# Optimization experiments

Hardware: AMD Instinct MI355X
Metric: run time of the kernel (lower is better)

The kernel has to match this reference:

```python
import jax, jax.numpy as jnp
import numpy as np

N_NODES = 50000
N_EDGES = 600000
IN_DIM = 4
HID = 128
N_LAYERS = 6
BN_EPS = 1e-5


def setup_inputs() -> dict:
    key = jax.random.key(0)
    ks = jax.random.split(key, 20)
    x = jax.random.normal(ks[0], (N_NODES, IN_DIM), dtype=jnp.float32)
    edge_index = jax.random.randint(ks[1], (2, N_EDGES), 0, N_NODES, dtype=jnp.int32)
    s = 0.05
    return {
        "x": x,
        "edge_index": edge_index,
        "enc_w": jax.random.normal(ks[2], (IN_DIM, HID), jnp.float32) * s,
        "enc_b": jnp.zeros((HID,), jnp.float32),
        "enc_bn_g": jnp.ones((HID,), jnp.float32),
        "enc_bn_b": jnp.zeros((HID,), jnp.float32),
        "conv_w": jax.random.normal(ks[3], (N_LAYERS, HID, HID), jnp.float32) * s,
        "conv_b": jnp.zeros((N_LAYERS, HID), jnp.float32),
        "bn_g": jnp.ones((N_LAYERS, HID), jnp.float32),
        "bn_b": jnp.zeros((N_LAYERS, HID), jnp.float32),
        "dec_w1": jax.random.normal(ks[4], (HID, HID // 2), jnp.float32) * s,
        "dec_b1": jnp.zeros((HID // 2,), jnp.float32),
        "dec_w2": jax.random.normal(ks[5], (HID // 2, HID // 4), jnp.float32) * s,
        "dec_b2": jnp.zeros((HID // 4,), jnp.float32),
        "dec_w3": jax.random.normal(ks[6], (HID // 4, 1), jnp.float32) * s,
        "dec_b3": jnp.zeros((1,), jnp.float32),
    }


def _batchnorm(h, g, b):
    # training-mode BatchNorm1d over node axis (biased variance, like torch)
    mu = h.mean(axis=0)
    var = jnp.mean(jnp.square(h - mu), axis=0)
    return (h - mu) * jax.lax.rsqrt(var + BN_EPS) * g + b


def _gcn_conv(h, W, b, src, dst, inv_sqrt_deg, n):
    # PyG GCNConv: sym-normalized A+I aggregation, aggregate at dst
    hw = h @ W                                   # [N, HID]
    norm = inv_sqrt_deg[src] * inv_sqrt_deg[dst]  # [E]
    msg = hw[src] * norm[:, None]                # [E, HID] (dominant traffic)
    agg = jax.ops.segment_sum(msg, dst, num_segments=n)
    self_loop = hw * jnp.square(inv_sqrt_deg)[:, None]
    return agg + self_loop + b


def reference(x, edge_index, enc_w, enc_b, enc_bn_g, enc_bn_b,
              conv_w, conv_b, bn_g, bn_b,
              dec_w1, dec_b1, dec_w2, dec_b2, dec_w3, dec_b3):
    n = x.shape[0]
    src, dst = edge_index[0], edge_index[1]
    # degree includes self loop (A + I)
    deg = jax.ops.segment_sum(jnp.ones_like(dst, dtype=x.dtype), dst, num_segments=n) + 1.0
    inv_sqrt_deg = jax.lax.rsqrt(deg)

    # encoder: Linear -> ReLU -> BatchNorm (dropout = identity in eval)
    h = jax.nn.relu(x @ enc_w + enc_b)
    h = _batchnorm(h, enc_bn_g, enc_bn_b)

    for l in range(N_LAYERS):
        h_new = _gcn_conv(h, conv_w[l], conv_b[l], src, dst, inv_sqrt_deg, n)
        h_new = jax.nn.relu(_batchnorm(h_new, bn_g[l], bn_b[l]))
        h = h + h_new  # residual

    # decoder MLP
    d = jax.nn.relu(h @ dec_w1 + dec_b1)
    d = jax.nn.relu(d @ dec_w2 + dec_b2)
    out = d @ dec_w3 + dec_b3
    return out.squeeze(-1)  # [N]
```

## Files before the change

### kernel.cpp

```cpp
#include <hip/hip_runtime.h>

#define BN_EPS 1e-5f

typedef unsigned int uint_t;
typedef unsigned short ushort_t;
typedef short bf16x8 __attribute__((ext_vector_type(8)));
typedef float f32x4 __attribute__((ext_vector_type(4)));

__device__ __forceinline__ float bflo(uint_t v) { return __uint_as_float(v << 16); }
__device__ __forceinline__ float bfhi(uint_t v) { return __uint_as_float(v & 0xffff0000u); }
__device__ __forceinline__ uint_t f2bf(float f) {
    uint_t u = __float_as_uint(f);
    u += 0x7fffu + ((u >> 16) & 1u);
    return u >> 16;
}

__device__ __forceinline__ void acc8(float* a, uint4 g, float w) {
    a[0] = fmaf(bflo(g.x), w, a[0]);
    a[1] = fmaf(bfhi(g.x), w, a[1]);
    a[2] = fmaf(bflo(g.y), w, a[2]);
    a[3] = fmaf(bfhi(g.y), w, a[3]);
    a[4] = fmaf(bflo(g.z), w, a[4]);
    a[5] = fmaf(bfhi(g.z), w, a[5]);
    a[6] = fmaf(bflo(g.w), w, a[6]);
    a[7] = fmaf(bfhi(g.w), w, a[7]);
}


__global__ void count_kernel(const int* __restrict__ ei, int* __restrict__ counts, int E) {
    int e = blockIdx.x * blockDim.x + threadIdx.x;
    if (e < E) atomicAdd(&counts[ei[E + e]], 1);
}

__global__ __launch_bounds__(256) void scan_part(const int* __restrict__ counts,
                                                 int* __restrict__ rowptr, int* __restrict__ bsum,
                                                 float* __restrict__ isd, int n) {
    const int tid = threadIdx.x;
    const int lane = tid & 63, wave = tid >> 6;
    __shared__ int wsum[4];
    int idx0 = blockIdx.x * 2048 + tid * 8;
    int v[8];
    int tsum = 0;
#pragma unroll
    for (int j = 0; j < 8; j++) {
        int i = idx0 + j;
        int c = (i < n) ? counts[i] : 0;
        if (i < n) isd[i] = rsqrtf((float)c + 1.0f);
        v[j] = (i < n) ? (((c + 4) >> 2) << 2) : 0;
        tsum += v[j];
    }
    int incl = tsum;
#pragma unroll
    for (int off = 1; off < 64; off <<= 1) {
        int t = __shfl_up(incl, off, 64);
        if (lane >= off) incl += t;
    }
    if (lane == 63) wsum[wave] = incl;
    __syncthreads();
    int wexcl = 0;
    for (int w2 = 0; w2 < wave; w2++) wexcl += wsum[w2];
    int run = wexcl + (incl - tsum);
#pragma unroll
    for (int j = 0; j < 8; j++) {
        int i = idx0 + j;
        if (i < n) rowptr[i] = run;
        run += v[j];
    }
    if (tid == 255) bsum[blockIdx.x] = run;
}

__global__ void scan_mid(int* __restrict__ bsum, int nb) {
    int lane = threadIdx.x;
    int v = (lane < nb) ? bsum[lane] : 0;
    int incl = v;
#pragma unroll
    for (int off = 1; off < 64; off <<= 1) {
        int t = __shfl_up(incl, off, 64);
        if (lane >= off) incl += t;
    }
    if (lane < nb) bsum[lane] = incl - v;
    if (lane == 63) bsum[nb] = incl;
}

__global__ void scan_add_self(int* __restrict__ rowptr, const int* __restrict__ bsum,
                              const int* __restrict__ counts, const float* __restrict__ isd,
                              int* __restrict__ cursor, int2* __restrict__ edges, int n, int nb) {
    int i = blockIdx.x * 256 + threadIdx.x;
    if (i < n) {
        int rp = rowptr[i] + bsum[i >> 11];
        rowptr[i] = rp;
        cursor[i] = rp;
        int c = counts[i];
        int pos = rp + c;
        int end = rp + (((c + 4) >> 2) << 2);
        float v = isd[i];
        edges[pos] = make_int2(i, __float_as_int(v * v));
        for (int p = pos + 1; p < end; p++) edges[p] = make_int2(i, 0);
    } else if (i == n) {
        rowptr[n] = bsum[nb];
    }
}

__global__ void scatter_kernel(const int* __restrict__ ei, int* __restrict__ cursor,
                               const float* __restrict__ isd, int2* __restrict__ edges, int E) {
    int e = blockIdx.x * blockDim.x + threadIdx.x;
    if (e < E) {
        int s = ei[e], d = ei[E + e];
        int idx = atomicAdd(&cursor[d], 1);
        edges[idx] = make_int2(s, __float_as_int(isd[s] * isd[d]));
    }
}


__global__ void wtrans_kernel(const float* __restrict__ W, ushort_t* __restrict__ Wt) {
    int id = blockIdx.x * 256 + threadIdx.x;
    int l = id >> 14, rem = id & 16383;
    int k = rem >> 7, n = rem & 127;
    Wt[(l << 14) + (n << 7) + k] = f2bf(W[id]);
}


__global__ __launch_bounds__(256) void encoder_kernel(const float* __restrict__ x,
                                                      const float* __restrict__ W,
                                                      const float* __restrict__ b,
                                                      float* __restrict__ h0,
                                                      float* __restrict__ stats, int N) {
    int tid = threadIdx.x;
    int g = blockIdx.x * 256 + tid;
    int total = gridDim.x * 256;
    int c = tid & 127;
    float w0 = W[c], w1 = W[128 + c], w2 = W[256 + c], w3 = W[384 + c], bb = b[c];
    float s = 0.f, q = 0.f;
    int tot = N * 128;
    for (int i = g; i < tot; i += total) {
        int n = i >> 7;
        float4 xv = ((const float4*)x)[n];
        float v = fmaf(xv.x, w0, fmaf(xv.y, w1, fmaf(xv.z, w2, fmaf(xv.w, w3, bb))));
        v = fmaxf(v, 0.f);
        h0[i] = v;
        s += v;
        q += v * v;
    }
    __shared__ float ls[256];
    ls[tid] = s;
    __syncthreads();
    if (tid < 128) atomicAdd(&stats[tid], ls[tid] + ls[tid + 128]);
    __syncthreads();
    ls[tid] = q;
    __syncthreads();
    if (tid < 128) atomicAdd(&stats[128 + tid], ls[tid] + ls[tid + 128]);
}


#define SWZ(byte, row) ((byte) ^ (((row) & 7) << 4))

template <int MODE>
__global__ __launch_bounds__(512) void mfma_gemm(const float* __restrict__ h,
                                                 const ushort_t* __restrict__ aggb,
                                                 const float* __restrict__ stats,
                                                 const float* __restrict__ g,
                                                 const float* __restrict__ beta, float invN,
                                                 const ushort_t* __restrict__ Wt,
                                                 float* __restrict__ hout,
                                                 ushort_t* __restrict__ hwb, int N) {
    __shared__ ushort_t As[128 * 128];
    __shared__ float s_sc[128], s_sh[128];
    const int tid = threadIdx.x;
    const int row0 = blockIdx.x * 128;

    if (tid < 128) {
        float S = stats[tid], Q = stats[tid + 128];
        float mu = S * invN;
        float var = fmaxf(Q * invN - mu * mu, 0.f);
        float rs = rsqrtf(var + BN_EPS);
        float sc = g[tid] * rs;
        s_sc[tid] = sc;
        s_sh[tid] = beta[tid] - mu * sc;
    }
    __syncthreads();

#pragma unroll
    for (int j = 0; j < 4; j++) {
        int idx = (j * 512 + tid) * 8;
        int r = idx >> 7, c = idx & 127;
        int grow = row0 + r;
        float av[8] = {0.f, 0.f, 0.f, 0.f, 0.f, 0.f, 0.f, 0.f};
        if (grow < N) {
            float4 h0 = *(const float4*)&h[(size_t)grow * 128 + c];
            float4 h1 = *(const float4*)&h[(size_t)grow * 128 + c + 4];
            float hv[8] = {h0.x, h0.y, h0.z, h0.w, h1.x, h1.y, h1.z, h1.w};
            if (MODE == 0) {
#pragma unroll
                for (int k = 0; k < 8; k++) av[k] = fmaf(hv[k], s_sc[c + k], s_sh[c + k]);
            } else {
                uint4 ag = *(const uint4*)&aggb[(size_t)grow * 128 + c];
                float ga[8] = {bflo(ag.x), bfhi(ag.x), bflo(ag.y), bfhi(ag.y),
                               bflo(ag.z), bfhi(ag.z), bflo(ag.w), bfhi(ag.w)};
#pragma unroll
                for (int k = 0; k < 8; k++)
                    av[k] = hv[k] + fmaxf(fmaf(ga[k], s_sc[c + k], s_sh[c + k]), 0.f);
            }
            *(float4*)&hout[(size_t)grow * 128 + c] = make_float4(av[0], av[1], av[2], av[3]);
            *(float4*)&hout[(size_t)grow * 128 + c + 4] = make_float4(av[4], av[5], av[6], av[7]);
        }
        uint4 p;
        p.x = f2bf(av[0]) | (f2bf(av[1]) << 16);
        p.y = f2bf(av[2]) | (f2bf(av[3]) << 16);
        p.z = f2bf(av[4]) | (f2bf(av[5]) << 16);
        p.w = f2bf(av[6]) | (f2bf(av[7]) << 16);
        *(uint4*)((char*)As + SWZ(r * 256 + c * 2, r)) = p;
    }
    __syncthreads();

    const int w = tid >> 6, l = tid & 63;
    const int mrow = l & 15, kg = l >> 4;
    const int arow = w * 16 + mrow;
    bf16x8 afr[4];
#pragma unroll
    for (int ks = 0; ks < 4; ks++)
        afr[ks] = *(const bf16x8*)((const char*)As + SWZ(arow * 256 + ks * 64 + kg * 16, arow));

    f32x4 acc[8];
#pragma unroll
    for (int nt = 0; nt < 8; nt++) acc[nt] = (f32x4){0.f, 0.f, 0.f, 0.f};

#pragma unroll
    for (int nt = 0; nt < 8; nt++) {
        const ushort_t* wp = &Wt[(size_t)(nt * 16 + mrow) * 128 + kg * 8];
#pragma unroll
        for (int ks = 0; ks < 4; ks++) {
            bf16x8 bfr = *(const bf16x8*)&wp[ks * 32];
            acc[nt] = __builtin_amdgcn_mfma_f32_16x16x32_bf16(afr[ks], bfr, acc[nt], 0, 0, 0);
        }
    }

#pragma unroll
    for (int nt = 0; nt < 8; nt++) {
#pragma unroll
        for (int r = 0; r < 4; r++) {
            int grow = row0 + w * 16 + kg * 4 + r;
            if (grow < N) hwb[(size_t)grow * 128 + nt * 16 + mrow] = f2bf(acc[nt][r]);
        }
    }
}


__global__ __launch_bounds__(256) void dec1_kernel(const float* __restrict__ A0,
                                                   const ushort_t* __restrict__ aggb,
                                                   const float* __restrict__ stats,
                                                   const float* __restrict__ g,
                                                   const float* __restrict__ beta, float invN,
                                                   const float* __restrict__ B,
                                                   const float* __restrict__ bias,
                                                   float* __restrict__ Cf, int N) {
    constexpr int K = 128, NOUT = 64, TN = NOUT / 16;
    constexpr int LDA = K + 1;
    __shared__ float As[64 * LDA];
    __shared__ float Bs[16 * NOUT];
    __shared__ float s_sc[128], s_sh[128];
    const int tid = threadIdx.x;
    const int row0 = blockIdx.x * 64;

    if (tid < 128) {
        float S = stats[tid], Q = stats[tid + 128];
        float mu = S * invN;
        float var = fmaxf(Q * invN - mu * mu, 0.f);
        float rs = rsqrtf(var + BN_EPS);
        float sc = g[tid] * rs;
        s_sc[tid] = sc;
        s_sh[tid] = beta[tid] - mu * sc;
    }
    __syncthreads();
#pragma unroll
    for (int j = 0; j < 4; j++) {
        int idx = (j * 256 + tid) * 8;
        int r = idx >> 7, c = idx & 127;
        int grow = row0 + r;
        float av[8] = {0.f, 0.f, 0.f, 0.f, 0.f, 0.f, 0.f, 0.f};
        if (grow < N) {
            float4 h0 = *(const float4*)&A0[(size_t)grow * 128 + c];
            float4 h1 = *(const float4*)&A0[(size_t)grow * 128 + c + 4];
            float hv[8] = {h0.x, h0.y, h0.z, h0.w, h1.x, h1.y, h1.z, h1.w};
            uint4 ag = *(const uint4*)&aggb[(size_t)grow * 128 + c];
            float ga[8] = {bflo(ag.x), bfhi(ag.x), bflo(ag.y), bfhi(ag.y),
                           bflo(ag.z), bfhi(ag.z), bflo(ag.w), bfhi(ag.w)};
#pragma unroll
            for (int k = 0; k < 8; k++)
                av[k] = hv[k] + fmaxf(fmaf(ga[k], s_sc[c + k], s_sh[c + k]), 0.f);
        }
#pragma unroll
        for (int k = 0; k < 8; k++) As[r * LDA + c + k] = av[k];
    }
    __syncthreads();

    float acc[4][TN];
#pragma unroll
    for (int i = 0; i < 4; i++)
#pragma unroll
        for (int j = 0; j < TN; j++) acc[i][j] = 0.f;

    const int tx = tid & 15, ty = tid >> 4;
    for (int k0 = 0; k0 < K; k0 += 16) {
        for (int f = tid; f < 16 * NOUT / 4; f += 256) {
            int r = f / (NOUT / 4), c4 = (f % (NOUT / 4)) * 4;
            *(float4*)&Bs[r * NOUT + c4] = *(const float4*)&B[(size_t)(k0 + r) * NOUT + c4];
        }
        __syncthreads();
#pragma unroll
        for (int kk = 0; kk < 16; ++kk) {
            float a[4], bf[TN];
#pragma unroll
            for (int i = 0; i < 4; i++) a[i] = As[(ty * 4 + i) * LDA + k0 + kk];
#pragma unroll
            for (int j = 0; j < TN; j++) bf[j] = Bs[kk * NOUT + tx * TN + j];
#pragma unroll
            for (int i = 0; i < 4; i++)
#pragma unroll
                for (int j = 0; j < TN; j++) acc[i][j] = fmaf(a[i], bf[j], acc[i][j]);
        }
        __syncthreads();
    }

#pragma unroll
    for (int i = 0; i < 4; i++) {
        int grow = row0 + ty * 4 + i;
        if (grow >= N) continue;
#pragma unroll
        for (int j = 0; j < TN; j++) {
            int c = tx * TN + j;
            Cf[(size_t)grow * NOUT + c] = fmaxf(acc[i][j] + bias[c], 0.f);
        }
    }
}


__global__ __launch_bounds__(256) void dec23_kernel(const float* __restrict__ d1,
                                                    const float* __restrict__ dw2,
                                                    const float* __restrict__ db2,
                                                    const float* __restrict__ dw3,
                                                    const float* __restrict__ db3,
                                                    float* __restrict__ out, int N) {
    constexpr int K = 64, NOUT = 32, TN = 2;
    __shared__ float As[64 * (K + 1)];
    __shared__ float Bs[K * NOUT];
    __shared__ float t2[64 * 33];
    __shared__ float w3s[32];
    const int tid = threadIdx.x;
    const int row0 = blockIdx.x * 64;

    if (tid < 32) w3s[tid] = dw3[tid];
#pragma unroll
    for (int j = 0; j < 4; j++) {
        int idx = (j * 256 + tid) * 4;
        int r = idx >> 6, c = idx & 63;
        int grow = row0 + r;
        float4 a = make_float4(0.f, 0.f, 0.f, 0.f);
        if (grow < N) a = *(const float4*)&d1[(size_t)grow * K + c];
        As[r * (K + 1) + c + 0] = a.x;
        As[r * (K + 1) + c + 1] = a.y;
        As[r * (K + 1) + c + 2] = a.z;
        As[r * (K + 1) + c + 3] = a.w;
    }
#pragma unroll
    for (int j = 0; j < 2; j++) {
        int f = (j * 256 + tid) * 4;
        *(float4*)&Bs[f] = *(const float4*)&dw2[f];
    }
    __syncthreads();

    const int tx = tid & 15, ty = tid >> 4;
    float acc[4][TN];
#pragma unroll
    for (int i = 0; i < 4; i++)
#pragma unroll
        for (int j = 0; j < TN; j++) acc[i][j] = 0.f;
#pragma unroll
    for (int kk = 0; kk < K; ++kk) {
        float a[4], bf[TN];
#pragma unroll
        for (int i = 0; i < 4; i++) a[i] = As[(ty * 4 + i) * (K + 1) + kk];
#pragma unroll
        for (int j = 0; j < TN; j++) bf[j] = Bs[kk * NOUT + tx * TN + j];
#pragma unroll
        for (int i = 0; i < 4; i++)
#pragma unroll
            for (int j = 0; j < TN; j++) acc[i][j] = fmaf(a[i], bf[j], acc[i][j]);
    }
#pragma unroll
    for (int i = 0; i < 4; i++) {
#pragma unroll
        for (int j = 0; j < TN; j++) {
            int c = tx * TN + j;
            t2[(ty * 4 + i) * 33 + c] = fmaxf(acc[i][j] + db2[c], 0.f);
        }
    }
    __syncthreads();
    if (tid < 64) {
        int n = row0 + tid;
        if (n < N) {
            float s = db3[0];
#pragma unroll
            for (int k = 0; k < 32; k++) s = fmaf(t2[tid * 33 + k], w3s[k], s);
            out[n] = s;
        }
    }
}


__global__ __launch_bounds__(256) void agg_kernel(const ushort_t* __restrict__ hwb,
                                                  const int* __restrict__ rowptr,
                                                  const int2* __restrict__ edges,
                                                  ushort_t* __restrict__ aggb,
                                                  float* __restrict__ stats, int N) {
    const int tid = threadIdx.x;
    const int wave = tid >> 6, lane = tid & 63;
    const int cbase = (lane & 15) * 8;
    const int gid = blockIdx.x * 16 + (tid >> 4);
    const int G = gridDim.x * 16;
    float s[8], q[8];
#pragma unroll
    for (int j = 0; j < 8; j++) {
        s[j] = 0.f;
        q[j] = 0.f;
    }

    for (int n = gid; n < N; n += G) {
        const int e0 = rowptr[n], e1 = rowptr[n + 1];
        float a[8] = {0.f, 0.f, 0.f, 0.f, 0.f, 0.f, 0.f, 0.f};
        for (int e = e0; e < e1; e += 16) {
            int c0 = min(e, e1 - 4);
            int c1 = min(e + 4, e1 - 4);
            int c2 = min(e + 8, e1 - 4);
            int c3 = min(e + 12, e1 - 4);
            int4 p0a = *(const int4*)&edges[c0];
            int4 p0b = *(const int4*)&edges[c0 + 2];
            int4 p1a = *(const int4*)&edges[c1];
            int4 p1b = *(const int4*)&edges[c1 + 2];
            int4 p2a = *(const int4*)&edges[c2];
            int4 p2b = *(const int4*)&edges[c2 + 2];
            int4 p3a = *(const int4*)&edges[c3];
            int4 p3b = *(const int4*)&edges[c3 + 2];
            float4 wv0 = make_float4(__int_as_float(p0a.y), __int_as_float(p0a.w),
                                     __int_as_float(p0b.y), __int_as_float(p0b.w));
            float4 wv1 = make_float4(__int_as_float(p1a.y), __int_as_float(p1a.w),
                                     __int_as_float(p1b.y), __int_as_float(p1b.w));
            float4 wv2 = make_float4(__int_as_float(p2a.y), __int_as_float(p2a.w),
                                     __int_as_float(p2b.y), __int_as_float(p2b.w));
            float4 wv3 = make_float4(__int_as_float(p3a.y), __int_as_float(p3a.w),
                                     __int_as_float(p3b.y), __int_as_float(p3b.w));
            if (e + 4 >= e1) wv1 = make_float4(0.f, 0.f, 0.f, 0.f);
            if (e + 8 >= e1) wv2 = make_float4(0.f, 0.f, 0.f, 0.f);
            if (e + 12 >= e1) wv3 = make_float4(0.f, 0.f, 0.f, 0.f);
            uint4 g0 = *(const uint4*)&hwb[(size_t)p0a.x * 128 + cbase];
            uint4 g1 = *(const uint4*)&hwb[(size_t)p0a.z * 128 + cbase];
            uint4 g2 = *(const uint4*)&hwb[(size_t)p0b.x * 128 + cbase];
            uint4 g3 = *(const uint4*)&hwb[(size_t)p0b.z * 128 + cbase];
            uint4 g4 = *(const uint4*)&hwb[(size_t)p1a.x * 128 + cbase];
            uint4 g5 = *(const uint4*)&hwb[(size_t)p1a.z * 128 + cbase];
            uint4 g6 = *(const uint4*)&hwb[(size_t)p1b.x * 128 + cbase];
            uint4 g7 = *(const uint4*)&hwb[(size_t)p1b.z * 128 + cbase];
            uint4 g8 = *(const uint4*)&hwb[(size_t)p2a.x * 128 + cbase];
            uint4 g9 = *(const uint4*)&hwb[(size_t)p2a.z * 128 + cbase];
            uint4 g10 = *(const uint4*)&hwb[(size_t)p2b.x * 128 + cbase];
            uint4 g11 = *(const uint4*)&hwb[(size_t)p2b.z * 128 + cbase];
            uint4 g12 = *(const uint4*)&hwb[(size_t)p3a.x * 128 + cbase];
            uint4 g13 = *(const uint4*)&hwb[(size_t)p3a.z * 128 + cbase];
            uint4 g14 = *(const uint4*)&hwb[(size_t)p3b.x * 128 + cbase];
            uint4 g15 = *(const uint4*)&hwb[(size_t)p3b.z * 128 + cbase];
            acc8(a, g0, wv0.x);
            acc8(a, g1, wv0.y);
            acc8(a, g2, wv0.z);
            acc8(a, g3, wv0.w);
            acc8(a, g4, wv1.x);
            acc8(a, g5, wv1.y);
            acc8(a, g6, wv1.z);
            acc8(a, g7, wv1.w);
            acc8(a, g8, wv2.x);
            acc8(a, g9, wv2.y);
            acc8(a, g10, wv2.z);
            acc8(a, g11, wv2.w);
            acc8(a, g12, wv3.x);
            acc8(a, g13, wv3.y);
            acc8(a, g14, wv3.z);
            acc8(a, g15, wv3.w);
        }
        uint4 p;
        p.x = f2bf(a[0]) | (f2bf(a[1]) << 16);
        p.y = f2bf(a[2]) | (f2bf(a[3]) << 16);
        p.z = f2bf(a[4]) | (f2bf(a[5]) << 16);
        p.w = f2bf(a[6]) | (f2bf(a[7]) << 16);
        *(uint4*)&aggb[(size_t)n * 128 + cbase] = p;
#pragma unroll
        for (int j = 0; j < 8; j++) {
            s[j] += a[j];
            q[j] += a[j] * a[j];
        }
    }

#pragma unroll
    for (int j = 0; j < 8; j++) {
        s[j] += __shfl_xor(s[j], 16, 64);
        s[j] += __shfl_xor(s[j], 32, 64);
        q[j] += __shfl_xor(q[j], 16, 64);
        q[j] += __shfl_xor(q[j], 32, 64);
    }
    __shared__ float ls[4][128];
    if (lane < 16) {
#pragma unroll
        for (int j = 0; j < 8; j++) ls[wave][cbase + j] = s[j];
    }
    __syncthreads();
    if (tid < 128) atomicAdd(&stats[tid], ls[0][tid] + ls[1][tid] + ls[2][tid] + ls[3][tid]);
    __syncthreads();
    if (lane < 16) {
#pragma unroll
        for (int j = 0; j < 8; j++) ls[wave][cbase + j] = q[j];
    }
    __syncthreads();
    if (tid < 128) atomicAdd(&stats[128 + tid], ls[0][tid] + ls[1][tid] + ls[2][tid] + ls[3][tid]);
}


extern "C" void kernel_launch(void* const* d_in, const int* in_sizes, int n_in, void* d_out,
                              int out_size, void* d_ws, size_t ws_size, hipStream_t stream) {
    const float* x = (const float*)d_in[0];
    const int* ei = (const int*)d_in[1];
    const float* enc_w = (const float*)d_in[2];
    const float* enc_b = (const float*)d_in[3];
    const float* enc_bn_g = (const float*)d_in[4];
    const float* enc_bn_b = (const float*)d_in[5];
    const float* conv_w = (const float*)d_in[6];
    const float* bn_g = (const float*)d_in[8];
    const float* bn_b = (const float*)d_in[9];
    const float* dw1 = (const float*)d_in[10];
    const float* db1 = (const float*)d_in[11];
    const float* dw2 = (const float*)d_in[12];
    const float* db2 = (const float*)d_in[13];
    const float* dw3 = (const float*)d_in[14];
    const float* db3 = (const float*)d_in[15];
    float* out = (float*)d_out;

    const int N = in_sizes[0] / 4;
    const int E = in_sizes[1] / 2;
    const size_t N128 = (size_t)N * 128;
    const float invN = 1.0f / N;

    float* h = (float*)d_ws;
    ushort_t* aggb = (ushort_t*)(h + N128);
    ushort_t* hwb = aggb + N128;
    ushort_t* wt = hwb + N128;
    float* stats = (float*)(wt + 6 * 16384);
    float* isd = stats + 7 * 256;
    int* counts = (int*)(isd + N);
    int* rowptr = counts + N;
    int* cursor = rowptr + N + 1;
    int* bsum = cursor + N;
    int2* edges = (int2*)(((uintptr_t)(bsum + 66) + 15) & ~(uintptr_t)15);
    float* d1 = (float*)hwb;
    float* d2 = (float*)aggb;

    (void)hipMemsetAsync(stats, 0, 7 * 256 * sizeof(float), stream);
    (void)hipMemsetAsync(counts, 0, (size_t)N * sizeof(int), stream);

    const int eb = (E + 255) / 256;
    const int snb = (N + 2047) / 2048;
    count_kernel<<<eb, 256, 0, stream>>>(ei, counts, E);
    scan_part<<<snb, 256, 0, stream>>>(counts, rowptr, bsum, isd, N);
    scan_mid<<<1, 64, 0, stream>>>(bsum, snb);
    scan_add_self<<<(N + 256) / 256, 256, 0, stream>>>(rowptr, bsum, counts, isd, cursor, edges,
                                                       N, snb);
    scatter_kernel<<<eb, 256, 0, stream>>>(ei, cursor, isd, edges, E);
    wtrans_kernel<<<384, 256, 0, stream>>>(conv_w, wt);

    encoder_kernel<<<1024, 256, 0, stream>>>(x, enc_w, enc_b, h, stats, N);

    const int mblocks = (N + 127) / 128;
    const int gblocks = (N + 63) / 64;
    const int ablocks = 768;

    mfma_gemm<0><<<mblocks, 512, 0, stream>>>(h, nullptr, stats, enc_bn_g, enc_bn_b, invN, wt, h,
                                              hwb, N);
    agg_kernel<<<ablocks, 256, 0, stream>>>(hwb, rowptr, edges, aggb, stats + 256, N);

    for (int l = 1; l < 6; l++) {
        mfma_gemm<1><<<mblocks, 512, 0, stream>>>(h, aggb, stats + l * 256, bn_g + (l - 1) * 128,
                                                  bn_b + (l - 1) * 128, invN,
                                                  wt + (size_t)l * 16384, h, hwb, N);
        agg_kernel<<<ablocks, 256, 0, stream>>>(hwb, rowptr, edges, aggb, stats + (l + 1) * 256,
                                                N);
    }

    dec1_kernel<<<gblocks, 256, 0, stream>>>(h, aggb, stats + 6 * 256, bn_g + 5 * 128,
                                             bn_b + 5 * 128, invN, dw1, db1, d1, N);
    dec23_kernel<<<gblocks, 256, 0, stream>>>(d1, dw2, db2, dw3, db3, out, N);
    (void)d2;
}
```

Baseline: 531.3 us.

## Fuse all GCN layer GEMM and aggregation stages into one cooperative persistent kernel

Replaces the twelve per-layer launches of the MFMA GEMM and aggregation kernels with a single cooperative kernel that loops over the six layers and uses grid-wide syncs between phases. The GEMM tile shrinks to 64 rows per 256-thread block and is processed in a grid-stride loop, and the aggregation runs in the same persistent blocks. The goal is to remove kernel launch gaps and tail effects. In exchange it adds grid.sync barriers, caps the grid by occupancy, and may lower per-phase parallelism or raise register pressure because two phases share one kernel.

New measurement: 1.403 ms. 164% more time.

```diff
diff --git a/kernel.cpp b/kernel.cpp
--- a/kernel.cpp
+++ b/kernel.cpp
@@ -1,4 +1,7 @@
 #include <hip/hip_runtime.h>
+#include <hip/hip_cooperative_groups.h>
+
+namespace cg = cooperative_groups;
 
 #define BN_EPS 1e-5f
 
@@ -110,7 +113,6 @@
         edges[idx] = make_int2(s, __float_as_int(isd[s] * isd[d]));
     }
 }
-
 
 __global__ void wtrans_kernel(const float* __restrict__ W, ushort_t* __restrict__ Wt) {
     int id = blockIdx.x * 256 + threadIdx.x;
@@ -154,93 +156,215 @@
 
 #define SWZ(byte, row) ((byte) ^ (((row) & 7) << 4))
 
-template <int MODE>
-__global__ __launch_bounds__(512) void mfma_gemm(const float* __restrict__ h,
-                                                 const ushort_t* __restrict__ aggb,
-                                                 const float* __restrict__ stats,
-                                                 const float* __restrict__ g,
-                                                 const float* __restrict__ beta, float invN,
-                                                 const ushort_t* __restrict__ Wt,
-                                                 float* __restrict__ hout,
-                                                 ushort_t* __restrict__ hwb, int N) {
-    __shared__ ushort_t As[128 * 128];
+__global__ __launch_bounds__(256, 4) void layers_kernel(
+    float* __restrict__ h, ushort_t* __restrict__ aggb, ushort_t* __restrict__ hwb,
+    const ushort_t* __restrict__ wt, float* __restrict__ stats, const float* __restrict__ enc_g,
+    const float* __restrict__ enc_bt, const float* __restrict__ bn_g,
+    const float* __restrict__ bn_b, const int* __restrict__ rowptr,
+    const int2* __restrict__ edges, float invN, int N) {
+    cg::grid_group grid = cg::this_grid();
+    __shared__ ushort_t As[64 * 128];
     __shared__ float s_sc[128], s_sh[128];
+    __shared__ float ls[4][128];
     const int tid = threadIdx.x;
-    const int row0 = blockIdx.x * 128;
-
-    if (tid < 128) {
-        float S = stats[tid], Q = stats[tid + 128];
-        float mu = S * invN;
-        float var = fmaxf(Q * invN - mu * mu, 0.f);
-        float rs = rsqrtf(var + BN_EPS);
-        float sc = g[tid] * rs;
-        s_sc[tid] = sc;
-        s_sh[tid] = beta[tid] - mu * sc;
-    }
-    __syncthreads();
-
-#pragma unroll
-    for (int j = 0; j < 4; j++) {
-        int idx = (j * 512 + tid) * 8;
-        int r = idx >> 7, c = idx & 127;
-        int grow = row0 + r;
-        float av[8] = {0.f, 0.f, 0.f, 0.f, 0.f, 0.f, 0.f, 0.f};
-        if (grow < N) {
-            float4 h0 = *(const float4*)&h[(size_t)grow * 128 + c];
-            float4 h1 = *(const float4*)&h[(size_t)grow * 128 + c + 4];
-            float hv[8] = {h0.x, h0.y, h0.z, h0.w, h1.x, h1.y, h1.z, h1.w};
-            if (MODE == 0) {
-#pragma unroll
-                for (int k = 0; k < 8; k++) av[k] = fmaf(hv[k], s_sc[c + k], s_sh[c + k]);
-            } else {
-                uint4 ag = *(const uint4*)&aggb[(size_t)grow * 128 + c];
-                float ga[8] = {bflo(ag.x), bfhi(ag.x), bflo(ag.y), bfhi(ag.y),
-                               bflo(ag.z), bfhi(ag.z), bflo(ag.w), bfhi(ag.w)};
-#pragma unroll
-                for (int k = 0; k < 8; k++)
-                    av[k] = hv[k] + fmaxf(fmaf(ga[k], s_sc[c + k], s_sh[c + k]), 0.f);
-            }
-            *(float4*)&hout[(size_t)grow * 128 + c] = make_float4(av[0], av[1], av[2], av[3]);
-            *(float4*)&hout[(size_t)grow * 128 + c + 4] = make_float4(av[4], av[5], av[6], av[7]);
-        }
-        uint4 p;
-        p.x = f2bf(av[0]) | (f2bf(av[1]) << 16);
-        p.y = f2bf(av[2]) | (f2bf(av[3]) << 16);
-        p.z = f2bf(av[4]) | (f2bf(av[5]) << 16);
-        p.w = f2bf(av[6]) | (f2bf(av[7]) << 16);
-        *(uint4*)((char*)As + SWZ(r * 256 + c * 2, r)) = p;
-    }
-    __syncthreads();
-
-    const int w = tid >> 6, l = tid & 63;
-    const int mrow = l & 15, kg = l >> 4;
-    const int arow = w * 16 + mrow;
-    bf16x8 afr[4];
-#pragma unroll
-    for (int ks = 0; ks < 4; ks++)
-        afr[ks] = *(const bf16x8*)((const char*)As + SWZ(arow * 256 + ks * 64 + kg * 16, arow));
-
-    f32x4 acc[8];
-#pragma unroll
-    for (int nt = 0; nt < 8; nt++) acc[nt] = (f32x4){0.f, 0.f, 0.f, 0.f};
-
-#pragma unroll
-    for (int nt = 0; nt < 8; nt++) {
-        const ushort_t* wp = &Wt[(size_t)(nt * 16 + mrow) * 128 + kg * 8];
-#pragma unroll
-        for (int ks = 0; ks < 4; ks++) {
-            bf16x8 bfr = *(const bf16x8*)&wp[ks * 32];
-            acc[nt] = __builtin_amdgcn_mfma_f32_16x16x32_bf16(afr[ks], bfr, acc[nt], 0, 0, 0);
-        }
-    }
-
-#pragma unroll
-    for (int nt = 0; nt < 8; nt++) {
-#pragma unroll
-        for (int r = 0; r < 4; r++) {
-            int grow = row0 + w * 16 + kg * 4 + r;
-            if (grow < N) hwb[(size_t)grow * 128 + nt * 16 + mrow] = f2bf(acc[nt][r]);
-        }
+    const int ntiles = (N + 63) >> 6;
+
+    for (int l = 0; l < 6; ++l) {
+        const float* stats_l = stats + l * 256;
+        const float* g = (l == 0) ? enc_g : bn_g + (l - 1) * 128;
+        const float* beta = (l == 0) ? enc_bt : bn_b + (l - 1) * 128;
+        const ushort_t* Wt = wt + (size_t)l * 16384;
+        if (tid < 128) {
+            float S = stats_l[tid], Q = stats_l[tid + 128];
+            float mu = S * invN;
+            float var = fmaxf(Q * invN - mu * mu, 0.f);
+            float rs = rsqrtf(var + BN_EPS);
+            float sc = g[tid] * rs;
+            s_sc[tid] = sc;
+            s_sh[tid] = beta[tid] - mu * sc;
+        }
+        __syncthreads();
+
+        for (int t = blockIdx.x; t < ntiles; t += gridDim.x) {
+            const int row0 = t << 6;
+#pragma unroll
+            for (int j = 0; j < 4; j++) {
+                int idx = (j * 256 + tid) * 8;
+                int r = idx >> 7, c = idx & 127;
+                int grow = row0 + r;
+                float av[8] = {0.f, 0.f, 0.f, 0.f, 0.f, 0.f, 0.f, 0.f};
+                if (grow < N) {
+                    float4 h0v = *(const float4*)&h[(size_t)grow * 128 + c];
+                    float4 h1v = *(const float4*)&h[(size_t)grow * 128 + c + 4];
+                    float hv[8] = {h0v.x, h0v.y, h0v.z, h0v.w, h1v.x, h1v.y, h1v.z, h1v.w};
+                    if (l == 0) {
+#pragma unroll
+                        for (int k = 0; k < 8; k++) av[k] = fmaf(hv[k], s_sc[c + k], s_sh[c + k]);
+                    } else {
+                        uint4 ag = *(const uint4*)&aggb[(size_t)grow * 128 + c];
+                        float ga[8] = {bflo(ag.x), bfhi(ag.x), bflo(ag.y), bfhi(ag.y),
+                                       bflo(ag.z), bfhi(ag.z), bflo(ag.w), bfhi(ag.w)};
+#pragma unroll
+                        for (int k = 0; k < 8; k++)
+                            av[k] = hv[k] + fmaxf(fmaf(ga[k], s_sc[c + k], s_sh[c + k]), 0.f);
+                    }
+                    *(float4*)&h[(size_t)grow * 128 + c] =
+                        make_float4(av[0], av[1], av[2], av[3]);
+                    *(float4*)&h[(size_t)grow * 128 + c + 4] =
+                        make_float4(av[4], av[5], av[6], av[7]);
+                }
+                uint4 p;
+                p.x = f2bf(av[0]) | (f2bf(av[1]) << 16);
+                p.y = f2bf(av[2]) | (f2bf(av[3]) << 16);
+                p.z = f2bf(av[4]) | (f2bf(av[5]) << 16);
+                p.w = f2bf(av[6]) | (f2bf(av[7]) << 16);
+                *(uint4*)((char*)As + SWZ(r * 256 + c * 2, r)) = p;
+            }
+            __syncthreads();
+
+            const int w = tid >> 6, lane = tid & 63;
+            const int mrow = lane & 15, kg = lane >> 4;
+            const int arow = w * 16 + mrow;
+            bf16x8 afr[4];
+#pragma unroll
+            for (int ks = 0; ks < 4; ks++)
+                afr[ks] =
+                    *(const bf16x8*)((const char*)As + SWZ(arow * 256 + ks * 64 + kg * 16, arow));
+
+            f32x4 acc[8];
+#pragma unroll
+            for (int nt = 0; nt < 8; nt++) acc[nt] = (f32x4){0.f, 0.f, 0.f, 0.f};
+#pragma unroll
+            for (int nt = 0; nt < 8; nt++) {
+                const ushort_t* wp = &Wt[(size_t)(nt * 16 + mrow) * 128 + kg * 8];
+#pragma unroll
+                for (int ks = 0; ks < 4; ks++) {
+                    bf16x8 bfr = *(const bf16x8*)&wp[ks * 32];
+                    acc[nt] =
+                        __builtin_amdgcn_mfma_f32_16x16x32_bf16(afr[ks], bfr, acc[nt], 0, 0, 0);
+                }
+            }
+#pragma unroll
+            for (int nt = 0; nt < 8; nt++) {
+#pragma unroll
+                for (int r = 0; r < 4; r++) {
+                    int grow = row0 + w * 16 + kg * 4 + r;
+                    if (grow < N) hwb[(size_t)grow * 128 + nt * 16 + mrow] = f2bf(acc[nt][r]);
+                }
+            }
+            __syncthreads();
+        }
+        grid.sync();
+
+        {
+            float* stats_n = stats + (l + 1) * 256;
+            const int wave = tid >> 6, lane = tid & 63;
+            const int cbase = (lane & 15) * 8;
+            const int gid = blockIdx.x * 16 + (tid >> 4);
+            const int G = gridDim.x * 16;
+            float s[8], q[8];
+#pragma unroll
+            for (int j = 0; j < 8; j++) {
+                s[j] = 0.f;
+                q[j] = 0.f;
+            }
+            for (int n = gid; n < N; n += G) {
+                const int e0 = rowptr[n], e1 = rowptr[n + 1];
+                float a[8] = {0.f, 0.f, 0.f, 0.f, 0.f, 0.f, 0.f, 0.f};
+                for (int e = e0; e < e1; e += 16) {
+                    int c0 = min(e, e1 - 4);
+                    int c1 = min(e + 4, e1 - 4);
+                    int c2 = min(e + 8, e1 - 4);
+                    int c3 = min(e + 12, e1 - 4);
+                    int4 p0a = *(const int4*)&edges[c0];
+                    int4 p0b = *(const int4*)&edges[c0 + 2];
+                    int4 p1a = *(const int4*)&edges[c1];
+                    int4 p1b = *(const int4*)&edges[c1 + 2];
+                    int4 p2a = *(const int4*)&edges[c2];
+                    int4 p2b = *(const int4*)&edges[c2 + 2];
+                    int4 p3a = *(const int4*)&edges[c3];
+                    int4 p3b = *(const int4*)&edges[c3 + 2];
+                    float4 wv0 = make_float4(__int_as_float(p0a.y), __int_as_float(p0a.w),
+                                             __int_as_float(p0b.y), __int_as_float(p0b.w));
+                    float4 wv1 = make_float4(__int_as_float(p1a.y), __int_as_float(p1a.w),
+                                             __int_as_float(p1b.y), __int_as_float(p1b.w));
+                    float4 wv2 = make_float4(__int_as_float(p2a.y), __int_as_float(p2a.w),
+                                             __int_as_float(p2b.y), __int_as_float(p2b.w));
+                    float4 wv3 = make_float4(__int_as_float(p3a.y), __int_as_float(p3a.w),
+                                             __int_as_float(p3b.y), __int_as_float(p3b.w));
+                    if (e + 4 >= e1) wv1 = make_float4(0.f, 0.f, 0.f, 0.f);
+                    if (e + 8 >= e1) wv2 = make_float4(0.f, 0.f, 0.f, 0.f);
+                    if (e + 12 >= e1) wv3 = make_float4(0.f, 0.f, 0.f, 0.f);
+                    uint4 g0 = *(const uint4*)&hwb[(size_t)p0a.x * 128 + cbase];
+                    uint4 g1 = *(const uint4*)&hwb[(size_t)p0a.z * 128 + cbase];
+                    uint4 g2 = *(const uint4*)&hwb[(size_t)p0b.x * 128 + cbase];
+                    uint4 g3 = *(const uint4*)&hwb[(size_t)p0b.z * 128 + cbase];
+                    uint4 g4 = *(const uint4*)&hwb[(size_t)p1a.x * 128 + cbase];
+                    uint4 g5 = *(const uint4*)&hwb[(size_t)p1a.z * 128 + cbase];
+                    uint4 g6 = *(const uint4*)&hwb[(size_t)p1b.x * 128 + cbase];
+                    uint4 g7 = *(const uint4*)&hwb[(size_t)p1b.z * 128 + cbase];
+                    uint4 g8 = *(const uint4*)&hwb[(size_t)p2a.x * 128 + cbase];
+                    uint4 g9 = *(const uint4*)&hwb[(size_t)p2a.z * 128 + cbase];
+                    uint4 g10 = *(const uint4*)&hwb[(size_t)p2b.x * 128 + cbase];
+                    uint4 g11 = *(const uint4*)&hwb[(size_t)p2b.z * 128 + cbase];
+                    uint4 g12 = *(const uint4*)&hwb[(size_t)p3a.x * 128 + cbase];
+                    uint4 g13 = *(const uint4*)&hwb[(size_t)p3a.z * 128 + cbase];
+                    uint4 g14 = *(const uint4*)&hwb[(size_t)p3b.x * 128 + cbase];
+                    uint4 g15 = *(const uint4*)&hwb[(size_t)p3b.z * 128 + cbase];
+                    acc8(a, g0, wv0.x);
+                    acc8(a, g1, wv0.y);
+                    acc8(a, g2, wv0.z);
+                    acc8(a, g3, wv0.w);
+                    acc8(a, g4, wv1.x);
+                    acc8(a, g5, wv1.y);
+                    acc8(a, g6, wv1.z);
+                    acc8(a, g7, wv1.w);
+                    acc8(a, g8, wv2.x);
+                    acc8(a, g9, wv2.y);
+                    acc8(a, g10, wv2.z);
+                    acc8(a, g11, wv2.w);
+                    acc8(a, g12, wv3.x);
+                    acc8(a, g13, wv3.y);
+                    acc8(a, g14, wv3.z);
+                    acc8(a, g15, wv3.w);
+                }
+                uint4 p;
+                p.x = f2bf(a[0]) | (f2bf(a[1]) << 16);
+                p.y = f2bf(a[2]) | (f2bf(a[3]) << 16);
+                p.z = f2bf(a[4]) | (f2bf(a[5]) << 16);
+                p.w = f2bf(a[6]) | (f2bf(a[7]) << 16);
+                *(uint4*)&aggb[(size_t)n * 128 + cbase] = p;
+#pragma unroll
+                for (int j = 0; j < 8; j++) {
+                    s[j] += a[j];
+                    q[j] += a[j] * a[j];
+                }
+            }
+#pragma unroll
+            for (int j = 0; j < 8; j++) {
+                s[j] += __shfl_xor(s[j], 16, 64);
+                s[j] += __shfl_xor(s[j], 32, 64);
+                q[j] += __shfl_xor(q[j], 16, 64);
+                q[j] += __shfl_xor(q[j], 32, 64);
+            }
+            __syncthreads();
+            if (lane < 16) {
+#pragma unroll
+                for (int j = 0; j < 8; j++) ls[wave][cbase + j] = s[j];
+            }
+            __syncthreads();
+            if (tid < 128)
+                atomicAdd(&stats_n[tid], ls[0][tid] + ls[1][tid] + ls[2][tid] + ls[3][tid]);
+            __syncthreads();
+            if (lane < 16) {
+#pragma unroll
+                for (int j = 0; j < 8; j++) ls[wave][cbase + j] = q[j];
+            }
+            __syncthreads();
+            if (tid < 128)
+                atomicAdd(&stats_n[128 + tid], ls[0][tid] + ls[1][tid] + ls[2][tid] + ls[3][tid]);
+        }
+        grid.sync();
     }
 }
 
@@ -404,120 +528,6 @@
             out[n] = s;
         }
     }
-}
-
-
-__global__ __launch_bounds__(256) void agg_kernel(const ushort_t* __restrict__ hwb,
-                                                  const int* __restrict__ rowptr,
-                                                  const int2* __restrict__ edges,
-                                                  ushort_t* __restrict__ aggb,
-                                                  float* __restrict__ stats, int N) {
-    const int tid = threadIdx.x;
-    const int wave = tid >> 6, lane = tid & 63;
-    const int cbase = (lane & 15) * 8;
-    const int gid = blockIdx.x * 16 + (tid >> 4);
-    const int G = gridDim.x * 16;
-    float s[8], q[8];
-#pragma unroll
-    for (int j = 0; j < 8; j++) {
-        s[j] = 0.f;
-        q[j] = 0.f;
-    }
-
-    for (int n = gid; n < N; n += G) {
-        const int e0 = rowptr[n], e1 = rowptr[n + 1];
-        float a[8] = {0.f, 0.f, 0.f, 0.f, 0.f, 0.f, 0.f, 0.f};
-        for (int e = e0; e < e1; e += 16) {
-            int c0 = min(e, e1 - 4);
-            int c1 = min(e + 4, e1 - 4);
-            int c2 = min(e + 8, e1 - 4);
-            int c3 = min(e + 12, e1 - 4);
-            int4 p0a = *(const int4*)&edges[c0];
-            int4 p0b = *(const int4*)&edges[c0 + 2];
-            int4 p1a = *(const int4*)&edges[c1];
-            int4 p1b = *(const int4*)&edges[c1 + 2];
-            int4 p2a = *(const int4*)&edges[c2];
-            int4 p2b = *(const int4*)&edges[c2 + 2];
-            int4 p3a = *(const int4*)&edges[c3];
-            int4 p3b = *(const int4*)&edges[c3 + 2];
-            float4 wv0 = make_float4(__int_as_float(p0a.y), __int_as_float(p0a.w),
-                                     __int_as_float(p0b.y), __int_as_float(p0b.w));
-            float4 wv1 = make_float4(__int_as_float(p1a.y), __int_as_float(p1a.w),
-                                     __int_as_float(p1b.y), __int_as_float(p1b.w));
-            float4 wv2 = make_float4(__int_as_float(p2a.y), __int_as_float(p2a.w),
-                                     __int_as_float(p2b.y), __int_as_float(p2b.w));
-            float4 wv3 = make_float4(__int_as_float(p3a.y), __int_as_float(p3a.w),
-                                     __int_as_float(p3b.y), __int_as_float(p3b.w));
-            if (e + 4 >= e1) wv1 = make_float4(0.f, 0.f, 0.f, 0.f);
-            if (e + 8 >= e1) wv2 = make_float4(0.f, 0.f, 0.f, 0.f);
-            if (e + 12 >= e1) wv3 = make_float4(0.f, 0.f, 0.f, 0.f);
-            uint4 g0 = *(const uint4*)&hwb[(size_t)p0a.x * 128 + cbase];
-            uint4 g1 = *(const uint4*)&hwb[(size_t)p0a.z * 128 + cbase];
-            uint4 g2 = *(const uint4*)&hwb[(size_t)p0b.x * 128 + cbase];
-            uint4 g3 = *(const uint4*)&hwb[(size_t)p0b.z * 128 + cbase];
-            uint4 g4 = *(const uint4*)&hwb[(size_t)p1a.x * 128 + cbase];
-            uint4 g5 = *(const uint4*)&hwb[(size_t)p1a.z * 128 + cbase];
-            uint4 g6 = *(const uint4*)&hwb[(size_t)p1b.x * 128 + cbase];
-            uint4 g7 = *(const uint4*)&hwb[(size_t)p1b.z * 128 + cbase];
-            uint4 g8 = *(const uint4*)&hwb[(size_t)p2a.x * 128 + cbase];
-            uint4 g9 = *(const uint4*)&hwb[(size_t)p2a.z * 128 + cbase];
-            uint4 g10 = *(const uint4*)&hwb[(size_t)p2b.x * 128 + cbase];
-            uint4 g11 = *(const uint4*)&hwb[(size_t)p2b.z * 128 + cbase];
-            uint4 g12 = *(const uint4*)&hwb[(size_t)p3a.x * 128 + cbase];
-            uint4 g13 = *(const uint4*)&hwb[(size_t)p3a.z * 128 + cbase];
-            uint4 g14 = *(const uint4*)&hwb[(size_t)p3b.x * 128 + cbase];
-            uint4 g15 = *(const uint4*)&hwb[(size_t)p3b.z * 128 + cbase];
-            acc8(a, g0, wv0.x);
-            acc8(a, g1, wv0.y);
-            acc8(a, g2, wv0.z);
-            acc8(a, g3, wv0.w);
-            acc8(a, g4, wv1.x);
-            acc8(a, g5, wv1.y);
-            acc8(a, g6, wv1.z);
-            acc8(a, g7, wv1.w);
-            acc8(a, g8, wv2.x);
-            acc8(a, g9, wv2.y);
-            acc8(a, g10, wv2.z);
-            acc8(a, g11, wv2.w);
-            acc8(a, g12, wv3.x);
-            acc8(a, g13, wv3.y);
-            acc8(a, g14, wv3.z);
-            acc8(a, g15, wv3.w);
-        }
-        uint4 p;
-        p.x = f2bf(a[0]) | (f2bf(a[1]) << 16);
-        p.y = f2bf(a[2]) | (f2bf(a[3]) << 16);
-        p.z = f2bf(a[4]) | (f2bf(a[5]) << 16);
-        p.w = f2bf(a[6]) | (f2bf(a[7]) << 16);
-        *(uint4*)&aggb[(size_t)n * 128 + cbase] = p;
-#pragma unroll
-        for (int j = 0; j < 8; j++) {
-            s[j] += a[j];
-            q[j] += a[j] * a[j];
-        }
-    }
-
-#pragma unroll
-    for (int j = 0; j < 8; j++) {
-        s[j] += __shfl_xor(s[j], 16, 64);
-        s[j] += __shfl_xor(s[j], 32, 64);
-        q[j] += __shfl_xor(q[j], 16, 64);
-        q[j] += __shfl_xor(q[j], 32, 64);
-    }
-    __shared__ float ls[4][128];
-    if (lane < 16) {
-#pragma unroll
-        for (int j = 0; j < 8; j++) ls[wave][cbase + j] = s[j];
-    }
-    __syncthreads();
-    if (tid < 128) atomicAdd(&stats[tid], ls[0][tid] + ls[1][tid] + ls[2][tid] + ls[3][tid]);
-    __syncthreads();
-    if (lane < 16) {
-#pragma unroll
-        for (int j = 0; j < 8; j++) ls[wave][cbase + j] = q[j];
-    }
-    __syncthreads();
-    if (tid < 128) atomicAdd(&stats[128 + tid], ls[0][tid] + ls[1][tid] + ls[2][tid] + ls[3][tid]);
 }
 
 
@@ -540,10 +550,10 @@
     const float* db3 = (const float*)d_in[15];
     float* out = (float*)d_out;
 
-    const int N = in_sizes[0] / 4;
+    int N = in_sizes[0] / 4;
     const int E = in_sizes[1] / 2;
     const size_t N128 = (size_t)N * 128;
-    const float invN = 1.0f / N;
+    float invN = 1.0f / N;
 
     float* h = (float*)d_ws;
     ushort_t* aggb = (ushort_t*)(h + N128);
@@ -557,7 +567,6 @@
     int* bsum = cursor + N;
     int2* edges = (int2*)(((uintptr_t)(bsum + 66) + 15) & ~(uintptr_t)15);
     float* d1 = (float*)hwb;
-    float* d2 = (float*)aggb;
 
     (void)hipMemsetAsync(stats, 0, 7 * 256 * sizeof(float), stream);
     (void)hipMemsetAsync(counts, 0, (size_t)N * sizeof(int), stream);
@@ -574,24 +583,22 @@
 
     encoder_kernel<<<1024, 256, 0, stream>>>(x, enc_w, enc_b, h, stats, N);
 
-    const int mblocks = (N + 127) / 128;
+    int maxb = 0;
+    if (hipOccupancyMaxActiveBlocksPerMultiprocessor(&maxb, (const void*)layers_kernel, 256, 0) !=
+            hipSuccess ||
+        maxb < 1)
+        maxb = 1;
+    int cgrid = maxb * 256;
+    if (cgrid > 1024) cgrid = 1024;
+    void* kargs[] = {(void*)&h,        (void*)&aggb, (void*)&hwb,    (void*)&wt,
+                     (void*)&stats,    (void*)&enc_bn_g, (void*)&enc_bn_b, (void*)&bn_g,
+                     (void*)&bn_b,     (void*)&rowptr,   (void*)&edges,    (void*)&invN,
+                     (void*)&N};
+    (void)hipLaunchCooperativeKernel((void*)layers_kernel, dim3(cgrid), dim3(256), kargs, 0,
+                                     stream);
+
     const int gblocks = (N + 63) / 64;
-    const int ablocks = 768;
-
-    mfma_gemm<0><<<mblocks, 512, 0, stream>>>(h, nullptr, stats, enc_bn_g, enc_bn_b, invN, wt, h,
-                                              hwb, N);
-    agg_kernel<<<ablocks, 256, 0, stream>>>(hwb, rowptr, edges, aggb, stats + 256, N);
-
-    for (int l = 1; l < 6; l++) {
-        mfma_gemm<1><<<mblocks, 512, 0, stream>>>(h, aggb, stats + l * 256, bn_g + (l - 1) * 128,
-                                                  bn_b + (l - 1) * 128, invN,
-                                                  wt + (size_t)l * 16384, h, hwb, N);
-        agg_kernel<<<ablocks, 256, 0, stream>>>(hwb, rowptr, edges, aggb, stats + (l + 1) * 256,
-                                                N);
-    }
-
     dec1_kernel<<<gblocks, 256, 0, stream>>>(h, aggb, stats + 6 * 256, bn_g + 5 * 128,
                                              bn_b + 5 * 128, invN, dw1, db1, d1, N);
     dec23_kernel<<<gblocks, 256, 0, stream>>>(d1, dw2, db2, dw3, db3, out, N);
-    (void)d2;
-}
+}
```
